# Performance work log

Measured on AMD Instinct MI355X. Metric: run time of the kernel, lower is better.

## Reference

```python
import jax, jax.numpy as jnp
import numpy as np


def setup_inputs() -> dict:
    key = jax.random.key(0)
    kq, kk, kv = jax.random.split(key, 3)
    B, N, H, D = 1, 4096, 16, 64
    q = jax.random.normal(kq, (B, N, H, D), dtype=jnp.float32)
    k = jax.random.normal(kk, (B, N, H, D), dtype=jnp.float32)
    v = jax.random.normal(kv, (B, N, H, D), dtype=jnp.float32)
    return {"q": q, "k": k, "v": v}


def reference(q, k, v):
    # q, k, v: [b, n, h, d]
    d = q.shape[-1]
    scale = 1.0 / jnp.sqrt(jnp.asarray(d, dtype=q.dtype))
    # scores: [b, h, n_q, n_k]
    scores = jnp.einsum("bqhd,bkhd->bhqk", q, k) * scale
    attn = jax.nn.softmax(scores, axis=-1)
    # output back in [b, n, h, d] layout
    out = jnp.einsum("bhqk,bkhd->bqhd", attn, v)
    return out
```

## Files before the change

kernel.cpp:

```cpp
#include <hip/hip_runtime.h>
#include <hip/hip_bf16.h>

#define H 16
#define D 64
#define NSEQ 4096
#define BM 256
#define BN 64
#define NT (NSEQ / BN)
#define NTH (NT / 2)

typedef __attribute__((ext_vector_type(8))) short bf16x8;
typedef __attribute__((ext_vector_type(4))) short short4v;
typedef __attribute__((ext_vector_type(4))) float f32x4;
typedef __attribute__((ext_vector_type(4))) float f4v;

union BF8 { bf16x8 v; unsigned u[4]; };
union S4  { short4v s; unsigned u[2]; };

static __device__ __forceinline__ unsigned pk2(float lo, float hi) {
    __hip_bfloat162 h = __float22bfloat162_rn(float2{lo, hi});
    unsigned u;
    __builtin_memcpy(&u, &h, 4);
    return u;
}

static __device__ __forceinline__ float fexp2(float x) {
#if __has_builtin(__builtin_amdgcn_exp2f)
    return __builtin_amdgcn_exp2f(x);
#else
    return exp2f(x);
#endif
}

#define TO_GBL(p) ((const __attribute__((address_space(1))) int*)(unsigned long long)(p))
#define TO_LDS(p) ((__attribute__((address_space(3))) int*)(unsigned int)(unsigned long long)(p))

__global__ void prep(const float* __restrict__ k, const float* __restrict__ v,
                     short* __restrict__ kb, short* __restrict__ vt) {
    __shared__ short L[64 * 72];
    const int h = blockIdx.y, n0 = blockIdx.x * 64, t = threadIdx.x;
    const int rw = t >> 4, c4 = (t & 15) * 4;
    #pragma unroll
    for (int it = 0; it < 4; ++it) {
        const int row = rw + it * 16;
        const size_t gro = ((size_t)(n0 + row) * H + h) * D + c4;
        f4v kf = *(const f4v*)(k + gro);
        S4 ks;
        ks.u[0] = pk2(kf[0], kf[1]);
        ks.u[1] = pk2(kf[2], kf[3]);
        *(short4v*)(kb + ((size_t)h * NSEQ + n0 + row) * D + c4) = ks.s;

        f4v vf = *(const f4v*)(v + gro);
        S4 vs;
        vs.u[0] = pk2(vf[0], vf[1]);
        vs.u[1] = pk2(vf[2], vf[3]);
        *(short4v*)&L[row * 72 + c4] = vs.s;
    }
    __syncthreads();
    const int tr = t & 15, tc = t >> 4;
    const int r0 = tr * 4, d0 = tc * 4;
    short4v ra[4];
    #pragma unroll
    for (int i = 0; i < 4; ++i) {
        const int s = r0 + i, s32 = s & 31, base32 = (s >> 5) * 32;
        const int phys = base32 + ((s32 >> 3) * 4 + (s32 & 3) + 16 * ((s32 >> 2) & 1));
        ra[i] = *(const short4v*)&L[phys * 72 + d0];
    }
    #pragma unroll
    for (int jj = 0; jj < 4; ++jj) {
        short4v o4 = (short4v){ra[0][jj], ra[1][jj], ra[2][jj], ra[3][jj]};
        *(short4v*)(vt + ((size_t)(h * D + d0 + jj)) * NSEQ + n0 + r0) = o4;
    }
}

__global__ __launch_bounds__(512, 2)
void attn_fwd(const float* __restrict__ q, const short* __restrict__ kb,
              const short* __restrict__ vtb, float* __restrict__ out)
{
    const int lin   = blockIdx.x;
    const int idx   = lin >> 3;
    const int h     = (lin & 7) * 2 + (idx >> 4);
    const int qbase = (idx & 15) * BM;

    const int tid   = threadIdx.x;
    const int wave  = tid >> 6;
    const int kg    = wave >> 2;
    const int qg    = wave & 3;
    const int lane  = tid & 63;
    const int lm    = lane & 15;
    const int quad  = lane >> 4;
    const int sw    = lm & 7;
    const int T0    = kg * NTH;

    __shared__ short Kt[2][4][BN * D];
    __shared__ short Vt[2][4][BN * D];

    const float c1 = 0.18033688011112042f;

    bf16x8 bq[4][2];
    #pragma unroll
    for (int g = 0; g < 4; ++g) {
        const int qrow = qbase + qg * 64 + g * 16 + lm;
        #pragma unroll
        for (int kc = 0; kc < 2; ++kc) {
            const float* qp = q + ((size_t)qrow * H + h) * D + kc * 32 + quad * 8;
            f4v q0 = *(const f4v*)qp;
            f4v q1 = *(const f4v*)(qp + 4);
            BF8 b;
            b.u[0] = pk2(q0[0] * c1, q0[1] * c1); b.u[1] = pk2(q0[2] * c1, q0[3] * c1);
            b.u[2] = pk2(q1[0] * c1, q1[1] * c1); b.u[3] = pk2(q1[2] * c1, q1[3] * c1);
            bq[g][kc] = b.v;
        }
    }

    BF8 ones;
    ones.u[0] = ones.u[1] = ones.u[2] = ones.u[3] = 0x3F803F80u;

    const f32x4 fz = (f32x4){0.f, 0.f, 0.f, 0.f};
    f32x4 o[4][4];
    #pragma unroll
    for (int g = 0; g < 4; ++g)
        #pragma unroll
        for (int mb = 0; mb < 4; ++mb) o[g][mb] = fz;
    f32x4 lacc[4];
    lacc[0] = fz; lacc[1] = fz; lacc[2] = fz; lacc[3] = fz;

    const int ci0 = (qg * 2 + 0) * 64 + lane;
    const int ci1 = (qg * 2 + 1) * 64 + lane;
    const int kr0 = ci0 >> 3, kp0 = (ci0 & 7) ^ (kr0 & 7);
    const int kr1 = ci1 >> 3, kp1 = (ci1 & 7) ^ (kr1 & 7);

    const short* kh = kb  + (size_t)h * NSEQ * D;
    const short* vh = vtb + (size_t)h * D * NSEQ;
    const short* pkA = kh + (size_t)(T0 * BN + kr0) * D + kp0 * 8;
    const short* pkB = kh + (size_t)(T0 * BN + kr1) * D + kp1 * 8;
    const short* pvA = vh + (size_t)kr0 * NSEQ + T0 * BN + kp0 * 8;
    const short* pvB = vh + (size_t)kr1 * NSEQ + T0 * BN + kp1 * 8;

    auto issue = [&](int b) {
        __builtin_amdgcn_global_load_lds(TO_GBL(pkA), TO_LDS(&Kt[kg][b][(qg * 2 + 0) * 512]), 16, 0, 0);
        __builtin_amdgcn_global_load_lds(TO_GBL(pkB), TO_LDS(&Kt[kg][b][(qg * 2 + 1) * 512]), 16, 0, 0);
        __builtin_amdgcn_global_load_lds(TO_GBL(pvA), TO_LDS(&Vt[kg][b][(qg * 2 + 0) * 512]), 16, 0, 0);
        __builtin_amdgcn_global_load_lds(TO_GBL(pvB), TO_LDS(&Vt[kg][b][(qg * 2 + 1) * 512]), 16, 0, 0);
        pkA += BN * D; pkB += BN * D; pvA += BN; pvB += BN;
    };

    const int posK0 = ((0 + quad) ^ sw) * 8;
    const int posK1 = ((4 + quad) ^ sw) * 8;

    auto compute = [&](int b) {
        const short* K_ = Kt[kg][b];
        const short* V_ = Vt[kg][b];

        bf16x8 kf0[4], kf1[4];
        #pragma unroll
        for (int nb = 0; nb < 4; ++nb) {
            kf0[nb] = *(const bf16x8*)&K_[(nb * 16 + lm) * 64 + posK0];
            kf1[nb] = *(const bf16x8*)&K_[(nb * 16 + lm) * 64 + posK1];
        }

        BF8 pb[4][2];
        #pragma unroll
        for (int g = 0; g < 4; ++g) {
            f32x4 st[4];
            #pragma unroll
            for (int nb = 0; nb < 4; ++nb) {
                st[nb] = __builtin_amdgcn_mfma_f32_16x16x32_bf16(kf0[nb], bq[g][0], fz, 0, 0, 0);
                st[nb] = __builtin_amdgcn_mfma_f32_16x16x32_bf16(kf1[nb], bq[g][1], st[nb], 0, 0, 0);
            }
            #pragma unroll
            for (int nb = 0; nb < 4; ++nb)
                #pragma unroll
                for (int r = 0; r < 4; ++r)
                    st[nb][r] = fexp2(st[nb][r]);
            #pragma unroll
            for (int c = 0; c < 2; ++c) {
                pb[g][c].u[0] = pk2(st[2 * c][0],     st[2 * c][1]);
                pb[g][c].u[1] = pk2(st[2 * c][2],     st[2 * c][3]);
                pb[g][c].u[2] = pk2(st[2 * c + 1][0], st[2 * c + 1][1]);
                pb[g][c].u[3] = pk2(st[2 * c + 1][2], st[2 * c + 1][3]);
            }
        }

        #pragma unroll
        for (int c = 0; c < 2; ++c)
            #pragma unroll
            for (int g = 0; g < 4; ++g)
                lacc[g] = __builtin_amdgcn_mfma_f32_16x16x32_bf16(ones.v, pb[g][c].v, lacc[g], 0, 0, 0);

        #pragma unroll
        for (int c = 0; c < 2; ++c) {
            const int pos = ((c * 4 + quad) ^ sw) * 8;
            #pragma unroll
            for (int mb = 0; mb < 4; ++mb) {
                bf16x8 vf = *(const bf16x8*)&V_[(mb * 16 + lm) * 64 + pos];
                #pragma unroll
                for (int g = 0; g < 4; ++g)
                    o[g][mb] = __builtin_amdgcn_mfma_f32_16x16x32_bf16(vf, pb[g][c].v, o[g][mb], 0, 0, 0);
            }
        }
    };

#define WAITV0 asm volatile("s_waitcnt vmcnt(0)" ::: "memory")
#define BARRIER() do { __builtin_amdgcn_s_barrier(); asm volatile("" ::: "memory"); } while (0)

    issue(0); issue(1);

    for (int k = 0; k < 7; ++k) {
        WAITV0; BARRIER();
        issue(2); issue(3);
        compute(0); compute(1);
        WAITV0; BARRIER();
        issue(0); issue(1);
        compute(2); compute(3);
    }
    WAITV0; BARRIER();
    issue(2); issue(3);
    compute(0); compute(1);
    WAITV0; BARRIER();
    compute(2); compute(3);

    float* Mo = (float*)&Kt[0][0][0];
    float* Ml = (float*)&Vt[0][0][0];
    const int slot = qg * 64 + lane;

    __syncthreads();
    if (kg == 1) {
        float* p = Mo + slot * 64;
        #pragma unroll
        for (int g = 0; g < 4; ++g)
            #pragma unroll
            for (int mb = 0; mb < 4; ++mb) {
                const int fi = g * 4 + mb;
                *(f32x4*)(p + ((fi ^ (slot & 15)) * 4)) = o[g][mb];
            }
        f32x4 lv = (f32x4){lacc[0][0], lacc[1][0], lacc[2][0], lacc[3][0]};
        *(f32x4*)(Ml + slot * 4) = lv;
    }
    __syncthreads();
    if (kg == 0) {
        const float* p = Mo + slot * 64;
        const f32x4 lv = *(const f32x4*)(Ml + slot * 4);
        #pragma unroll
        for (int g = 0; g < 4; ++g) {
            const float inv = 1.0f / (lacc[g][0] + lv[g]);
            const int qrow = qbase + qg * 64 + g * 16 + lm;
            float* op = out + ((size_t)qrow * H + h) * D + quad * 4;
            #pragma unroll
            for (int mb = 0; mb < 4; ++mb) {
                const int fi = g * 4 + mb;
                const f32x4 ob = *(const f32x4*)(p + ((fi ^ (slot & 15)) * 4));
                f4v w;
                #pragma unroll
                for (int r = 0; r < 4; ++r) w[r] = (o[g][mb][r] + ob[r]) * inv;
                *(f4v*)(op + mb * 16) = w;
            }
        }
    }
}

extern "C" void kernel_launch(void* const* d_in, const int* in_sizes, int n_in,
                              void* d_out, int out_size, void* d_ws, size_t ws_size,
                              hipStream_t stream) {
    const float* q = (const float*)d_in[0];
    const float* k = (const float*)d_in[1];
    const float* v = (const float*)d_in[2];
    float* out = (float*)d_out;

    short* kb = (short*)d_ws;
    short* vt = kb + (size_t)H * NSEQ * D;

    prep<<<dim3(NSEQ / 64, H), dim3(256), 0, stream>>>(k, v, kb, vt);
    attn_fwd<<<dim3((NSEQ / BM) * H * 2 / 2), dim3(512), 0, stream>>>(q, kb, vt, out);
}
```

Before: 163.4 us.

## Halve query tile to 128 rows with 4-wave blocks and a simpler double-buffered loop

The query tile shrinks from 256 to 128 rows and each block drops from 8 waves to 4 (2 key groups × 2 query groups). The grid doubles to 512 blocks, so the GPU can hold two independent blocks per CU instead of one. Each wave now issues four K and four V async loads per tile. The software pipeline is reduced from two tiles in flight to a plain double buffer, one tile ahead. The aim is better latency hiding through independent blocks and less barrier coupling, at the cost of twice as much K/V traffic per query and a shallower prefetch.

```diff
diff --git a/kernel.cpp b/kernel.cpp
--- a/kernel.cpp
+++ b/kernel.cpp
@@ -4,7 +4,7 @@
 #define H 16
 #define D 64
 #define NSEQ 4096
-#define BM 256
+#define BM 128
 #define BN 64
 #define NT (NSEQ / BN)
 #define NTH (NT / 2)
@@ -73,27 +73,27 @@
     }
 }
 
-__global__ __launch_bounds__(512, 2)
+__global__ __launch_bounds__(256, 2)
 void attn_fwd(const float* __restrict__ q, const short* __restrict__ kb,
               const short* __restrict__ vtb, float* __restrict__ out)
 {
     const int lin   = blockIdx.x;
     const int idx   = lin >> 3;
-    const int h     = (lin & 7) * 2 + (idx >> 4);
-    const int qbase = (idx & 15) * BM;
+    const int h     = (lin & 7) * 2 + (idx >> 5);
+    const int qbase = (idx & 31) * BM;
 
     const int tid   = threadIdx.x;
     const int wave  = tid >> 6;
-    const int kg    = wave >> 2;
-    const int qg    = wave & 3;
+    const int kg    = wave >> 1;
+    const int qg    = wave & 1;
     const int lane  = tid & 63;
     const int lm    = lane & 15;
     const int quad  = lane >> 4;
     const int sw    = lm & 7;
     const int T0    = kg * NTH;
 
-    __shared__ short Kt[2][4][BN * D];
-    __shared__ short Vt[2][4][BN * D];
+    __shared__ short Kt[2][2][BN * D];
+    __shared__ short Vt[2][2][BN * D];
 
     const float c1 = 0.18033688011112042f;
 
@@ -125,24 +125,39 @@
     f32x4 lacc[4];
     lacc[0] = fz; lacc[1] = fz; lacc[2] = fz; lacc[3] = fz;
 
-    const int ci0 = (qg * 2 + 0) * 64 + lane;
-    const int ci1 = (qg * 2 + 1) * 64 + lane;
+    const int ci0 = qg * 256 + 0 * 64 + lane;
+    const int ci1 = qg * 256 + 1 * 64 + lane;
+    const int ci2 = qg * 256 + 2 * 64 + lane;
+    const int ci3 = qg * 256 + 3 * 64 + lane;
     const int kr0 = ci0 >> 3, kp0 = (ci0 & 7) ^ (kr0 & 7);
     const int kr1 = ci1 >> 3, kp1 = (ci1 & 7) ^ (kr1 & 7);
+    const int kr2 = ci2 >> 3, kp2 = (ci2 & 7) ^ (kr2 & 7);
+    const int kr3 = ci3 >> 3, kp3 = (ci3 & 7) ^ (kr3 & 7);
 
     const short* kh = kb  + (size_t)h * NSEQ * D;
     const short* vh = vtb + (size_t)h * D * NSEQ;
-    const short* pkA = kh + (size_t)(T0 * BN + kr0) * D + kp0 * 8;
-    const short* pkB = kh + (size_t)(T0 * BN + kr1) * D + kp1 * 8;
-    const short* pvA = vh + (size_t)kr0 * NSEQ + T0 * BN + kp0 * 8;
-    const short* pvB = vh + (size_t)kr1 * NSEQ + T0 * BN + kp1 * 8;
+    const short* pk0 = kh + (size_t)(T0 * BN + kr0) * D + kp0 * 8;
+    const short* pk1 = kh + (size_t)(T0 * BN + kr1) * D + kp1 * 8;
+    const short* pk2_ = kh + (size_t)(T0 * BN + kr2) * D + kp2 * 8;
+    const short* pk3 = kh + (size_t)(T0 * BN + kr3) * D + kp3 * 8;
+    const short* pv0 = vh + (size_t)kr0 * NSEQ + T0 * BN + kp0 * 8;
+    const short* pv1 = vh + (size_t)kr1 * NSEQ + T0 * BN + kp1 * 8;
+    const short* pv2 = vh + (size_t)kr2 * NSEQ + T0 * BN + kp2 * 8;
+    const short* pv3 = vh + (size_t)kr3 * NSEQ + T0 * BN + kp3 * 8;
 
     auto issue = [&](int b) {
-        __builtin_amdgcn_global_load_lds(TO_GBL(pkA), TO_LDS(&Kt[kg][b][(qg * 2 + 0) * 512]), 16, 0, 0);
-        __builtin_amdgcn_global_load_lds(TO_GBL(pkB), TO_LDS(&Kt[kg][b][(qg * 2 + 1) * 512]), 16, 0, 0);
-        __builtin_amdgcn_global_load_lds(TO_GBL(pvA), TO_LDS(&Vt[kg][b][(qg * 2 + 0) * 512]), 16, 0, 0);
-        __builtin_amdgcn_global_load_lds(TO_GBL(pvB), TO_LDS(&Vt[kg][b][(qg * 2 + 1) * 512]), 16, 0, 0);
-        pkA += BN * D; pkB += BN * D; pvA += BN; pvB += BN;
+        short* kd = &Kt[kg][b][qg * 2048];
+        short* vd = &Vt[kg][b][qg * 2048];
+        __builtin_amdgcn_global_load_lds(TO_GBL(pk0), TO_LDS(kd +    0), 16, 0, 0);
+        __builtin_amdgcn_global_load_lds(TO_GBL(pk1), TO_LDS(kd +  512), 16, 0, 0);
+        __builtin_amdgcn_global_load_lds(TO_GBL(pk2_), TO_LDS(kd + 1024), 16, 0, 0);
+        __builtin_amdgcn_global_load_lds(TO_GBL(pk3), TO_LDS(kd + 1536), 16, 0, 0);
+        __builtin_amdgcn_global_load_lds(TO_GBL(pv0), TO_LDS(vd +    0), 16, 0, 0);
+        __builtin_amdgcn_global_load_lds(TO_GBL(pv1), TO_LDS(vd +  512), 16, 0, 0);
+        __builtin_amdgcn_global_load_lds(TO_GBL(pv2), TO_LDS(vd + 1024), 16, 0, 0);
+        __builtin_amdgcn_global_load_lds(TO_GBL(pv3), TO_LDS(vd + 1536), 16, 0, 0);
+        pk0 += BN * D; pk1 += BN * D; pk2_ += BN * D; pk3 += BN * D;
+        pv0 += BN; pv1 += BN; pv2 += BN; pv3 += BN;
     };
 
     const int posK0 = ((0 + quad) ^ sw) * 8;
@@ -204,21 +219,14 @@
 #define WAITV0 asm volatile("s_waitcnt vmcnt(0)" ::: "memory")
 #define BARRIER() do { __builtin_amdgcn_s_barrier(); asm volatile("" ::: "memory"); } while (0)
 
-    issue(0); issue(1);
-
-    for (int k = 0; k < 7; ++k) {
+    issue(0);
+    for (int t = 0; t < NTH - 1; ++t) {
         WAITV0; BARRIER();
-        issue(2); issue(3);
-        compute(0); compute(1);
-        WAITV0; BARRIER();
-        issue(0); issue(1);
-        compute(2); compute(3);
+        issue((t + 1) & 1);
+        compute(t & 1);
     }
     WAITV0; BARRIER();
-    issue(2); issue(3);
-    compute(0); compute(1);
-    WAITV0; BARRIER();
-    compute(2); compute(3);
+    compute((NTH - 1) & 1);
 
     float* Mo = (float*)&Kt[0][0][0];
     float* Ml = (float*)&Vt[0][0][0];
@@ -271,5 +279,5 @@
     short* vt = kb + (size_t)H * NSEQ * D;
 
     prep<<<dim3(NSEQ / 64, H), dim3(256), 0, stream>>>(k, v, kb, vt);
-    attn_fwd<<<dim3((NSEQ / BM) * H * 2 / 2), dim3(512), 0, stream>>>(q, kb, vt, out);
-}
+    attn_fwd<<<dim3((NSEQ / BM) * H), dim3(256), 0, stream>>>(q, kb, vt, out);
+}
```

Result: no change. 165.4 us (+1.2%).
